# Kernel tuning notes

Measured on AMD Instinct MI355X. Metric: run time of the kernel, lower is better.

The kernel has to match this reference:

```python
import jax, jax.numpy as jnp
import numpy as np

# Instant-NGP style multiresolution hash grid config
L = 16                      # n_levels
F = 2                       # n_feat_per_entry
LEVEL_SIZE = 524288         # 2^19 hash entries per level
RES = np.array([16, 22, 30, 42, 58, 80, 111, 154, 212, 294, 406, 561, 776, 1072, 1482, 2048], np.int32)
OFFSETS = (np.arange(L + 1) * LEVEL_SIZE).astype(np.int32)
PRIMES = np.array([1, 2654435761, 805459861], dtype=np.uint32)  # spatial hash primes
# 8 corner offsets of a voxel, (8, 3) in {0,1}
CORNERS = np.array([[(c >> d) & 1 for d in range(3)] for c in range(8)], np.int32)


def setup_inputs() -> dict:
    key = jax.random.key(0)
    k1, k2 = jax.random.split(key)
    B = 1000000
    xyz = jax.random.uniform(k1, (B, 3), dtype=jnp.float32)  # points in [0,1)
    embeddings = jax.random.normal(k2, (int(OFFSETS[-1]), F), dtype=jnp.float32) * 0.01
    return {
        'xyz': xyz,
        'embeddings': embeddings,
        'min_xyz': jnp.zeros((3,), jnp.float32),
        'max_xyz': jnp.ones((3,), jnp.float32),
    }


def _encode(xyz, embeddings, min_xyz, max_xyz):
    B = xyz.shape[0]
    norm = (xyz - min_xyz) / (max_xyz - min_xyz)          # (B, 3) in [0,1] if inside grid
    valid = jnp.all((norm >= 0.0) & (norm <= 1.0), axis=-1)  # (B,)
    corners = jnp.asarray(CORNERS)                        # (8, 3)
    primes = jnp.asarray(PRIMES)
    outs = []
    for l in range(L):  # fixed small loop over levels (different resolution per level)
        r = int(RES[l])
        pos = norm * (r - 1)                              # (B, 3) grid coords
        fi = jnp.clip(jnp.floor(pos).astype(jnp.int32), 0, r - 2)  # (B, 3) base corner
        frac = pos - fi.astype(pos.dtype)                 # (B, 3) trilinear fraction
        c = fi[:, None, :] + corners[None, :, :]          # (B, 8, 3) corner coords
        # trilinear interpolation weights, (B, 8)
        w = jnp.prod(jnp.where(corners[None] == 1, frac[:, None, :], 1.0 - frac[:, None, :]), axis=-1)
        # spatial hash into this level's table slice
        cu = c.astype(jnp.uint32)
        h = (cu[..., 0] * primes[0]) ^ (cu[..., 1] * primes[1]) ^ (cu[..., 2] * primes[2])
        lvl_size = jnp.uint32(int(OFFSETS[l + 1] - OFFSETS[l]))
        idx = (h % lvl_size).astype(jnp.int32) + int(OFFSETS[l])   # (B, 8) global entry ids
        feats = embeddings[idx]                           # (B, 8, F) irregular gather
        outs.append(jnp.sum(w[..., None] * feats, axis=1))  # (B, F)
    out = jnp.stack(outs, axis=1).reshape(B, L * F)       # (B, L*F)
    return jnp.where(valid[:, None], out, jnp.zeros((), out.dtype))


def reference(xyz, embeddings, min_xyz, max_xyz):
    return _encode(xyz, embeddings, min_xyz, max_xyz)
```

## Files before the change

kernel.cpp:

```cpp
#include <hip/hip_runtime.h>
#include <hip/hip_fp16.h>
#include <stdint.h>

#define NLEVELS 16
#define BLOCK 256
#define NPT 2

#define P1 2654435761u
#define P2 805459861u
#define HMASK 0x7FFFFu

__device__ __host__ constexpr int DRES(int l) {
    constexpr int r[6] = {16, 22, 30, 42, 58, 80};
    return r[l];
}
__device__ __host__ constexpr uint32_t QOFF(int l) {
    constexpr uint32_t o[7] = {0, 3600, 13302, 38532, 109134, 297576, 796856};
    return o[l];
}
#define QUAD_ENTRIES 796856u
#define HASH16_ENTRIES (10u << 19)
#define HASH16_BYTES ((size_t)HASH16_ENTRIES * 4)
#define QUAD_BYTES   ((size_t)QUAD_ENTRIES * 16)
#define PREP_TOTAL   (HASH16_ENTRIES + QUAD_ENTRIES)


__device__ __forceinline__ uint32_t fetch_pack(const float* __restrict__ emb,
                                               int l, uint32_t x, uint32_t y, uint32_t z)
{
    const uint32_t h = (x ^ (y * P1) ^ (z * P2)) & HMASK;
    const float2 v = *reinterpret_cast<const float2*>(emb + (((size_t)l << 19) + h) * 2);
    __half2 hv = __floats2half2_rn(v.x, v.y);
    return *reinterpret_cast<uint32_t*>(&hv);
}

template <int L>
__device__ __forceinline__ void qbuild(uint32_t rel, const float* __restrict__ emb,
                                       uint4* __restrict__ quad)
{
    constexpr int r = DRES(L);
    constexpr int rW = r - 1;
    const uint32_t fz = rel / (uint32_t)(rW * rW);
    const uint32_t rem = rel - fz * (uint32_t)(rW * rW);
    const uint32_t fy = rem / (uint32_t)rW;
    const uint32_t fx = rem - fy * (uint32_t)rW;
    uint4 q;
    q.x = fetch_pack(emb, L, fx,     fy,     fz);
    q.y = fetch_pack(emb, L, fx + 1, fy,     fz);
    q.z = fetch_pack(emb, L, fx,     fy + 1, fz);
    q.w = fetch_pack(emb, L, fx + 1, fy + 1, fz);
    quad[QOFF(L) + rel] = q;
}

__global__ __launch_bounds__(BLOCK) void prep_kernel(
    const float* __restrict__ emb,
    uint32_t* __restrict__ tab16,
    uint4* __restrict__ quad)
{
    const uint32_t i = blockIdx.x * BLOCK + threadIdx.x;
    if (i < HASH16_ENTRIES) {
        const float2 v = *reinterpret_cast<const float2*>(
            emb + (((size_t)(6u << 19)) + i) * 2);
        __half2 hv = __floats2half2_rn(v.x, v.y);
        __builtin_nontemporal_store(*reinterpret_cast<uint32_t*>(&hv), &tab16[i]);
    } else if (i < PREP_TOTAL) {
        const uint32_t j = i - HASH16_ENTRIES;
        if      (j < QOFF(1)) qbuild<0>(j - QOFF(0), emb, quad);
        else if (j < QOFF(2)) qbuild<1>(j - QOFF(1), emb, quad);
        else if (j < QOFF(3)) qbuild<2>(j - QOFF(2), emb, quad);
        else if (j < QOFF(4)) qbuild<3>(j - QOFF(3), emb, quad);
        else if (j < QOFF(5)) qbuild<4>(j - QOFF(4), emb, quad);
        else                  qbuild<5>(j - QOFF(5), emb, quad);
    }
}


struct PointCtx { float nx, ny, nz; bool valid; };

__device__ __forceinline__ PointCtx make_ctx(const float* __restrict__ xyz, int pt, int B,
                                             float mn0, float mn1, float mn2,
                                             float inv0, float inv1, float inv2)
{
    PointCtx P;
    P.nx = P.ny = P.nz = 0.0f;
    P.valid = false;
    if (pt < B) {
        const float x = xyz[3 * pt + 0];
        const float y = xyz[3 * pt + 1];
        const float z = xyz[3 * pt + 2];
        P.nx = (x - mn0) * inv0;
        P.ny = (y - mn1) * inv1;
        P.nz = (z - mn2) * inv2;
        P.valid = (P.nx >= 0.0f) && (P.nx <= 1.0f) &&
                  (P.ny >= 0.0f) && (P.ny <= 1.0f) &&
                  (P.nz >= 0.0f) && (P.nz <= 1.0f);
    }
    return P;
}

__device__ __forceinline__ void frac_setup(const PointCtx& P, int r,
                                           int& fx, int& fy, int& fz,
                                           float& wx0, float& wx1,
                                           float& wy0, float& wy1,
                                           float& wz0, float& wz1)
{
    const float rm1 = (float)(r - 1);
    const float px = P.nx * rm1, py = P.ny * rm1, pz = P.nz * rm1;
    fx = (int)floorf(px); fx = min(max(fx, 0), r - 2);
    fy = (int)floorf(py); fy = min(max(fy, 0), r - 2);
    fz = (int)floorf(pz); fz = min(max(fz, 0), r - 2);
    wx1 = px - (float)fx; wx0 = 1.0f - wx1;
    wy1 = py - (float)fy; wy0 = 1.0f - wy1;
    wz1 = pz - (float)fz; wz0 = 1.0f - wz1;
}

__device__ __forceinline__ float2 h2f(uint32_t e)
{
    return __half22float2(*reinterpret_cast<const __half2*>(&e));
}

__device__ __forceinline__ float2 quad_encode(const PointCtx& P, int r, uint32_t qoff,
                                              const uint4* __restrict__ quad)
{
    int fx, fy, fz; float wx0, wx1, wy0, wy1, wz0, wz1;
    frac_setup(P, r, fx, fy, fz, wx0, wx1, wy0, wy1, wz0, wz1);
    const int rW = r - 1;
    const uint32_t base = qoff + (uint32_t)(fx + fy * rW + fz * rW * rW);
    const uint4 q0 = quad[base];
    const uint4 q1 = quad[base + (uint32_t)(rW * rW)];

    const float2 a0 = h2f(q0.x), b0 = h2f(q0.y), c0 = h2f(q0.z), d0 = h2f(q0.w);
    const float2 a1 = h2f(q1.x), b1 = h2f(q1.y), c1 = h2f(q1.z), d1 = h2f(q1.w);

    const float p0x = wy0 * (wx0 * a0.x + wx1 * b0.x) + wy1 * (wx0 * c0.x + wx1 * d0.x);
    const float p0y = wy0 * (wx0 * a0.y + wx1 * b0.y) + wy1 * (wx0 * c0.y + wx1 * d0.y);
    const float p1x = wy0 * (wx0 * a1.x + wx1 * b1.x) + wy1 * (wx0 * c1.x + wx1 * d1.x);
    const float p1y = wy0 * (wx0 * a1.y + wx1 * b1.y) + wy1 * (wx0 * c1.y + wx1 * d1.y);

    float2 o;
    o.x = P.valid ? (wz0 * p0x + wz1 * p1x) : 0.0f;
    o.y = P.valid ? (wz0 * p0y + wz1 * p1y) : 0.0f;
    return o;
}

__device__ __forceinline__ float2 hash_encode(const PointCtx& P, int r,
                                              const uint32_t* __restrict__ lt)
{
    int fx, fy, fz; float wx0, wx1, wy0, wy1, wz0, wz1;
    frac_setup(P, r, fx, fy, fz, wx0, wx1, wy0, wy1, wz0, wz1);
    const uint32_t hx0 = (uint32_t)fx;
    const uint32_t hy0 = (uint32_t)fy * P1, hy1 = hy0 + P1;
    const uint32_t hz0 = (uint32_t)fz * P2, hz1 = hz0 + P2;
    const bool oddx = (fx & 1) != 0;

    uint32_t i0[4];
    uint2 pr[4];
    #pragma unroll
    for (int yz = 0; yz < 4; ++yz) {
        const uint32_t rest = ((yz & 1) ? hy1 : hy0) ^ ((yz & 2) ? hz1 : hz0);
        i0[yz] = (hx0 ^ rest) & HMASK;
        pr[yz] = *reinterpret_cast<const uint2*>(lt + (i0[yz] & ~1u));
    }
    uint32_t e1x[4] = {0, 0, 0, 0};
    if (oddx) {
        #pragma unroll
        for (int yz = 0; yz < 4; ++yz) {
            const uint32_t rest = ((yz & 1) ? hy1 : hy0) ^ ((yz & 2) ? hz1 : hz0);
            e1x[yz] = lt[((hx0 + 1u) ^ rest) & HMASK];
        }
    }

    float acc0 = 0.0f, acc1 = 0.0f;
    #pragma unroll
    for (int yz = 0; yz < 4; ++yz) {
        const float wyz = ((yz & 1) ? wy1 : wy0) * ((yz & 2) ? wz1 : wz0);
        const uint32_t eA = (i0[yz] & 1u) ? pr[yz].y : pr[yz].x;
        const uint32_t eB0 = (i0[yz] & 1u) ? pr[yz].x : pr[yz].y;
        const uint32_t eB = oddx ? e1x[yz] : eB0;
        const float2 cA = h2f(eA);
        const float2 cB = h2f(eB);
        acc0 += wyz * (wx0 * cA.x + wx1 * cB.x);
        acc1 += wyz * (wx0 * cA.y + wx1 * cB.y);
    }
    float2 o;
    o.x = P.valid ? acc0 : 0.0f;
    o.y = P.valid ? acc1 : 0.0f;
    return o;
}

__device__ __forceinline__ void nt_store_f2h(uint32_t* p, float2 v)
{
    __half2 h = __floats2half2_rn(v.x, v.y);
    __builtin_nontemporal_store(*reinterpret_cast<uint32_t*>(&h), p);
}

__global__ __launch_bounds__(BLOCK, 4) void gather_mega_kernel(
    const float* __restrict__ xyz,
    const uint32_t* __restrict__ tab16,
    const uint4* __restrict__ quad,
    const float* __restrict__ minv,
    const float* __restrict__ maxv,
    uint32_t* __restrict__ slab,
    int B, int blocks2)
{
    constexpr int HRES[10] = {111, 154, 212, 294, 406, 561, 776, 1072, 1482, 2048};

    const int seg = blockIdx.x / blocks2;
    const int blk = blockIdx.x - seg * blocks2;

    const int t = threadIdx.x;
    const int p0 = blk * (NPT * BLOCK) + t;
    const int p1 = p0 + BLOCK;

    const float mn0 = minv[0], mn1 = minv[1], mn2 = minv[2];
    const float inv0 = 1.0f / (maxv[0] - mn0);
    const float inv1 = 1.0f / (maxv[1] - mn1);
    const float inv2 = 1.0f / (maxv[2] - mn2);

    const PointCtx A  = make_ctx(xyz, p0, B, mn0, mn1, mn2, inv0, inv1, inv2);
    const PointCtx Bc = make_ctx(xyz, p1, B, mn0, mn1, mn2, inv0, inv1, inv2);

    if (seg == 0) {
        #pragma unroll
        for (int l = 0; l < 5; ++l) {
            const float2 o0 = quad_encode(A,  DRES(l), QOFF(l), quad);
            const float2 o1 = quad_encode(Bc, DRES(l), QOFF(l), quad);
            if (p0 < B) nt_store_f2h(&slab[(size_t)l * B + p0], o0);
            if (p1 < B) nt_store_f2h(&slab[(size_t)l * B + p1], o1);
        }
    } else if (seg == 1) {
        const float2 o0 = quad_encode(A,  DRES(5), QOFF(5), quad);
        const float2 o1 = quad_encode(Bc, DRES(5), QOFF(5), quad);
        if (p0 < B) nt_store_f2h(&slab[(size_t)5 * B + p0], o0);
        if (p1 < B) nt_store_f2h(&slab[(size_t)5 * B + p1], o1);
    } else {
        const int l = seg + 4;
        const int r = HRES[seg - 2];
        const uint32_t* __restrict__ lt = tab16 + ((size_t)(l - 6) << 19);
        const float2 o0 = hash_encode(A,  r, lt);
        const float2 o1 = hash_encode(Bc, r, lt);
        if (p0 < B) nt_store_f2h(&slab[(size_t)l * B + p0], o0);
        if (p1 < B) nt_store_f2h(&slab[(size_t)l * B + p1], o1);
    }
}

__global__ __launch_bounds__(BLOCK) void transpose_kernel(
    const uint32_t* __restrict__ slab,
    float* __restrict__ out,
    int B)
{
    __shared__ float s[32][BLOCK + 1];
    const int t = threadIdx.x;
    const int pt = blockIdx.x * BLOCK + t;

    #pragma unroll
    for (int l = 0; l < NLEVELS; ++l) {
        float2 v = make_float2(0.0f, 0.0f);
        if (pt < B) {
            const uint32_t bits = __builtin_nontemporal_load(&slab[(size_t)l * B + pt]);
            v = h2f(bits);
        }
        s[2 * l + 0][t] = v.x;
        s[2 * l + 1][t] = v.y;
    }
    __syncthreads();

    const size_t chunk = (size_t)blockIdx.x * (BLOCK * 32);
    const size_t total = (size_t)B * 32;
    #pragma unroll
    for (int k = 0; k < 32; ++k) {
        const int flat = k * BLOCK + t;
        const int p = flat >> 5;
        const int c = flat & 31;
        const size_t g = chunk + (size_t)flat;
        if (g < total) __builtin_nontemporal_store(s[c][p], &out[g]);
    }
}

__global__ __launch_bounds__(BLOCK) void hashgrid_fused_kernel(
    const float* __restrict__ xyz,
    const float* __restrict__ emb,
    const float* __restrict__ minv,
    const float* __restrict__ maxv,
    float* __restrict__ out,
    int B)
{
    constexpr int RES[NLEVELS] = {16, 22, 30, 42, 58, 80, 111, 154,
                                  212, 294, 406, 561, 776, 1072, 1482, 2048};
    __shared__ float s[32][BLOCK + 1];
    const int t = threadIdx.x;
    const int pt = blockIdx.x * BLOCK + t;

    const float mn0 = minv[0], mn1 = minv[1], mn2 = minv[2];
    const float inv0 = 1.0f / (maxv[0] - mn0);
    const float inv1 = 1.0f / (maxv[1] - mn1);
    const float inv2 = 1.0f / (maxv[2] - mn2);

    const PointCtx P = make_ctx(xyz, pt, B, mn0, mn1, mn2, inv0, inv1, inv2);

    #pragma unroll
    for (int l = 0; l < NLEVELS; ++l) {
        int fx, fy, fz; float wx0, wx1, wy0, wy1, wz0, wz1;
        frac_setup(P, RES[l], fx, fy, fz, wx0, wx1, wy0, wy1, wz0, wz1);
        const uint32_t hx0 = (uint32_t)fx, hx1 = hx0 + 1u;
        const uint32_t hy0 = (uint32_t)fy * P1, hy1 = hy0 + P1;
        const uint32_t hz0 = (uint32_t)fz * P2, hz1 = hz0 + P2;
        const float* __restrict__ lemb = emb + ((size_t)l << 20);
        float acc0 = 0.0f, acc1 = 0.0f;
        #pragma unroll
        for (int k = 0; k < 8; ++k) {
            const uint32_t h = (((k & 1) ? hx1 : hx0) ^
                                ((k & 2) ? hy1 : hy0) ^
                                ((k & 4) ? hz1 : hz0)) & HMASK;
            const float2 f = *reinterpret_cast<const float2*>(lemb + ((size_t)h << 1));
            const float w = ((k & 1) ? wx1 : wx0) * ((k & 2) ? wy1 : wy0) * ((k & 4) ? wz1 : wz0);
            acc0 = fmaf(w, f.x, acc0);
            acc1 = fmaf(w, f.y, acc1);
        }
        s[2 * l + 0][t] = P.valid ? acc0 : 0.0f;
        s[2 * l + 1][t] = P.valid ? acc1 : 0.0f;
    }
    __syncthreads();
    const size_t chunk = (size_t)blockIdx.x * (BLOCK * 32);
    const size_t total = (size_t)B * 32;
    #pragma unroll
    for (int k = 0; k < 32; ++k) {
        const int flat = k * BLOCK + t;
        const int p = flat >> 5;
        const int c = flat & 31;
        const size_t g = chunk + (size_t)flat;
        if (g < total) out[g] = s[c][p];
    }
}

extern "C" void kernel_launch(void* const* d_in, const int* in_sizes, int n_in,
                              void* d_out, int out_size, void* d_ws, size_t ws_size,
                              hipStream_t stream) {
    const float* xyz = (const float*)d_in[0];
    const float* emb = (const float*)d_in[1];
    const float* mn  = (const float*)d_in[2];
    const float* mx  = (const float*)d_in[3];
    float* out = (float*)d_out;

    const int B = in_sizes[0] / 3;
    const int blocks1 = (B + BLOCK - 1) / BLOCK;
    const int blocks2 = (B + NPT * BLOCK - 1) / (NPT * BLOCK);

    const size_t slab_bytes = (size_t)NLEVELS * (size_t)B * 4;
    const size_t ws_needed = slab_bytes + HASH16_BYTES + QUAD_BYTES;

    if (ws_size >= ws_needed) {
        uint32_t* slab  = (uint32_t*)d_ws;
        uint32_t* tab16 = (uint32_t*)((char*)d_ws + slab_bytes);
        uint4*    quad  = (uint4*)((char*)d_ws + slab_bytes + HASH16_BYTES);

        hipLaunchKernelGGL(prep_kernel,
                           dim3((PREP_TOTAL + BLOCK - 1) / BLOCK), dim3(BLOCK),
                           0, stream, emb, tab16, quad);

        hipLaunchKernelGGL(gather_mega_kernel, dim3(12 * blocks2), dim3(BLOCK), 0, stream,
                           xyz, tab16, quad, mn, mx, slab, B, blocks2);

        hipLaunchKernelGGL(transpose_kernel, dim3(blocks1), dim3(BLOCK), 0, stream,
                           slab, out, B);
    } else {
        hipLaunchKernelGGL(hashgrid_fused_kernel, dim3(blocks1), dim3(BLOCK), 0, stream,
                           xyz, emb, mn, mx, out, B);
    }
}
```

Measured before the change: 368.5 us.

## Replace quad-packed dense tables with x-pair duplicated tables and simplify hash gather

Dense levels 0-5 now store one 8-byte x-pair record per voxel (two fp16x2 corner features) instead of 16-byte quads covering the x/y face. Interpolation therefore needs four 8-byte loads per point instead of two 16-byte loads, and the precomputed table is about half the size. The hash levels drop the paired-load and odd-x trick in favour of eight plain 4-byte gathers. The smaller dense table cuts prep writes, at the cost of more load instructions in the gather kernel.

```diff
diff --git a/kernel.cpp b/kernel.cpp
--- a/kernel.cpp
+++ b/kernel.cpp
@@ -14,15 +14,15 @@
     constexpr int r[6] = {16, 22, 30, 42, 58, 80};
     return r[l];
 }
-__device__ __host__ constexpr uint32_t QOFF(int l) {
-    constexpr uint32_t o[7] = {0, 3600, 13302, 38532, 109134, 297576, 796856};
+__device__ __host__ constexpr uint32_t DOFF(int l) {
+    constexpr uint32_t o[7] = {0, 4096, 14744, 41744, 115832, 310944, 822944};
     return o[l];
 }
-#define QUAD_ENTRIES 796856u
+#define DENSE_ENTRIES 822944u
 #define HASH16_ENTRIES (10u << 19)
 #define HASH16_BYTES ((size_t)HASH16_ENTRIES * 4)
-#define QUAD_BYTES   ((size_t)QUAD_ENTRIES * 16)
-#define PREP_TOTAL   (HASH16_ENTRIES + QUAD_ENTRIES)
+#define DUP_BYTES    ((size_t)DENSE_ENTRIES * 8)
+#define PREP_TOTAL   (HASH16_ENTRIES + DENSE_ENTRIES)
 
 
 __device__ __forceinline__ uint32_t fetch_pack(const float* __restrict__ emb,
@@ -34,28 +34,10 @@
     return *reinterpret_cast<uint32_t*>(&hv);
 }
 
-template <int L>
-__device__ __forceinline__ void qbuild(uint32_t rel, const float* __restrict__ emb,
-                                       uint4* __restrict__ quad)
-{
-    constexpr int r = DRES(L);
-    constexpr int rW = r - 1;
-    const uint32_t fz = rel / (uint32_t)(rW * rW);
-    const uint32_t rem = rel - fz * (uint32_t)(rW * rW);
-    const uint32_t fy = rem / (uint32_t)rW;
-    const uint32_t fx = rem - fy * (uint32_t)rW;
-    uint4 q;
-    q.x = fetch_pack(emb, L, fx,     fy,     fz);
-    q.y = fetch_pack(emb, L, fx + 1, fy,     fz);
-    q.z = fetch_pack(emb, L, fx,     fy + 1, fz);
-    q.w = fetch_pack(emb, L, fx + 1, fy + 1, fz);
-    quad[QOFF(L) + rel] = q;
-}
-
 __global__ __launch_bounds__(BLOCK) void prep_kernel(
     const float* __restrict__ emb,
     uint32_t* __restrict__ tab16,
-    uint4* __restrict__ quad)
+    uint2* __restrict__ dup)
 {
     const uint32_t i = blockIdx.x * BLOCK + threadIdx.x;
     if (i < HASH16_ENTRIES) {
@@ -65,12 +47,20 @@
         __builtin_nontemporal_store(*reinterpret_cast<uint32_t*>(&hv), &tab16[i]);
     } else if (i < PREP_TOTAL) {
         const uint32_t j = i - HASH16_ENTRIES;
-        if      (j < QOFF(1)) qbuild<0>(j - QOFF(0), emb, quad);
-        else if (j < QOFF(2)) qbuild<1>(j - QOFF(1), emb, quad);
-        else if (j < QOFF(3)) qbuild<2>(j - QOFF(2), emb, quad);
-        else if (j < QOFF(4)) qbuild<3>(j - QOFF(3), emb, quad);
-        else if (j < QOFF(5)) qbuild<4>(j - QOFF(4), emb, quad);
-        else                  qbuild<5>(j - QOFF(5), emb, quad);
+        int l = 0;
+        #pragma unroll
+        for (int q = 1; q < 6; ++q) if (j >= DOFF(q)) l = q;
+        const int r = DRES(l);
+        const uint32_t rel = j - DOFF(l);
+        const uint32_t z = rel / (uint32_t)(r * r);
+        const uint32_t rem = rel - z * (uint32_t)(r * r);
+        const uint32_t y = rem / (uint32_t)r;
+        const uint32_t x = rem - y * (uint32_t)r;
+        const uint32_t x1 = min(x + 1u, (uint32_t)(r - 1));
+        uint2 e;
+        e.x = fetch_pack(emb, l, x,  y, z);
+        e.y = fetch_pack(emb, l, x1, y, z);
+        dup[j] = e;
     }
 }
 
@@ -119,68 +109,42 @@
     return __half22float2(*reinterpret_cast<const __half2*>(&e));
 }
 
-__device__ __forceinline__ float2 quad_encode(const PointCtx& P, int r, uint32_t qoff,
-                                              const uint4* __restrict__ quad)
+__device__ __forceinline__ float2 dup_encode(const PointCtx& P, int r, uint32_t off,
+                                             const uint2* __restrict__ dup)
 {
     int fx, fy, fz; float wx0, wx1, wy0, wy1, wz0, wz1;
     frac_setup(P, r, fx, fy, fz, wx0, wx1, wy0, wy1, wz0, wz1);
-    const int rW = r - 1;
-    const uint32_t base = qoff + (uint32_t)(fx + fy * rW + fz * rW * rW);
-    const uint4 q0 = quad[base];
-    const uint4 q1 = quad[base + (uint32_t)(rW * rW)];
-
-    const float2 a0 = h2f(q0.x), b0 = h2f(q0.y), c0 = h2f(q0.z), d0 = h2f(q0.w);
-    const float2 a1 = h2f(q1.x), b1 = h2f(q1.y), c1 = h2f(q1.z), d1 = h2f(q1.w);
-
-    const float p0x = wy0 * (wx0 * a0.x + wx1 * b0.x) + wy1 * (wx0 * c0.x + wx1 * d0.x);
-    const float p0y = wy0 * (wx0 * a0.y + wx1 * b0.y) + wy1 * (wx0 * c0.y + wx1 * d0.y);
-    const float p1x = wy0 * (wx0 * a1.x + wx1 * b1.x) + wy1 * (wx0 * c1.x + wx1 * d1.x);
-    const float p1y = wy0 * (wx0 * a1.y + wx1 * b1.y) + wy1 * (wx0 * c1.y + wx1 * d1.y);
-
-    float2 o;
-    o.x = P.valid ? (wz0 * p0x + wz1 * p1x) : 0.0f;
-    o.y = P.valid ? (wz0 * p0y + wz1 * p1y) : 0.0f;
-    return o;
-}
-
-__device__ __forceinline__ float2 hash_encode(const PointCtx& P, int r,
-                                              const uint32_t* __restrict__ lt)
-{
-    int fx, fy, fz; float wx0, wx1, wy0, wy1, wz0, wz1;
-    frac_setup(P, r, fx, fy, fz, wx0, wx1, wy0, wy1, wz0, wz1);
-    const uint32_t hx0 = (uint32_t)fx;
-    const uint32_t hy0 = (uint32_t)fy * P1, hy1 = hy0 + P1;
-    const uint32_t hz0 = (uint32_t)fz * P2, hz1 = hz0 + P2;
-    const bool oddx = (fx & 1) != 0;
-
-    uint32_t i0[4];
-    uint2 pr[4];
-    #pragma unroll
-    for (int yz = 0; yz < 4; ++yz) {
-        const uint32_t rest = ((yz & 1) ? hy1 : hy0) ^ ((yz & 2) ? hz1 : hz0);
-        i0[yz] = (hx0 ^ rest) & HMASK;
-        pr[yz] = *reinterpret_cast<const uint2*>(lt + (i0[yz] & ~1u));
-    }
-    uint32_t e1x[4] = {0, 0, 0, 0};
-    if (oddx) {
-        #pragma unroll
-        for (int yz = 0; yz < 4; ++yz) {
-            const uint32_t rest = ((yz & 1) ? hy1 : hy0) ^ ((yz & 2) ? hz1 : hz0);
-            e1x[yz] = lt[((hx0 + 1u) ^ rest) & HMASK];
-        }
-    }
+    const uint32_t base = off + (uint32_t)(fx + fy * r + fz * r * r);
+
+    const uint2 q00 = dup[base];
+    const uint2 q10 = dup[base + (uint32_t)r];
+    const uint2 q01 = dup[base + (uint32_t)(r * r)];
+    const uint2 q11 = dup[base + (uint32_t)(r + r * r)];
 
     float acc0 = 0.0f, acc1 = 0.0f;
-    #pragma unroll
-    for (int yz = 0; yz < 4; ++yz) {
-        const float wyz = ((yz & 1) ? wy1 : wy0) * ((yz & 2) ? wz1 : wz0);
-        const uint32_t eA = (i0[yz] & 1u) ? pr[yz].y : pr[yz].x;
-        const uint32_t eB0 = (i0[yz] & 1u) ? pr[yz].x : pr[yz].y;
-        const uint32_t eB = oddx ? e1x[yz] : eB0;
-        const float2 cA = h2f(eA);
-        const float2 cB = h2f(eB);
-        acc0 += wyz * (wx0 * cA.x + wx1 * cB.x);
-        acc1 += wyz * (wx0 * cA.y + wx1 * cB.y);
+    {
+        const float w = wy0 * wz0;
+        const float2 a = h2f(q00.x), b = h2f(q00.y);
+        acc0 += w * (wx0 * a.x + wx1 * b.x);
+        acc1 += w * (wx0 * a.y + wx1 * b.y);
+    }
+    {
+        const float w = wy1 * wz0;
+        const float2 a = h2f(q10.x), b = h2f(q10.y);
+        acc0 += w * (wx0 * a.x + wx1 * b.x);
+        acc1 += w * (wx0 * a.y + wx1 * b.y);
+    }
+    {
+        const float w = wy0 * wz1;
+        const float2 a = h2f(q01.x), b = h2f(q01.y);
+        acc0 += w * (wx0 * a.x + wx1 * b.x);
+        acc1 += w * (wx0 * a.y + wx1 * b.y);
+    }
+    {
+        const float w = wy1 * wz1;
+        const float2 a = h2f(q11.x), b = h2f(q11.y);
+        acc0 += w * (wx0 * a.x + wx1 * b.x);
+        acc1 += w * (wx0 * a.y + wx1 * b.y);
     }
     float2 o;
     o.x = P.valid ? acc0 : 0.0f;
@@ -188,6 +152,37 @@
     return o;
 }
 
+__device__ __forceinline__ float2 hash_encode(const PointCtx& P, int r,
+                                              const uint32_t* __restrict__ lt)
+{
+    int fx, fy, fz; float wx0, wx1, wy0, wy1, wz0, wz1;
+    frac_setup(P, r, fx, fy, fz, wx0, wx1, wy0, wy1, wz0, wz1);
+    const uint32_t hx0 = (uint32_t)fx,      hx1 = hx0 + 1u;
+    const uint32_t hy0 = (uint32_t)fy * P1, hy1 = hy0 + P1;
+    const uint32_t hz0 = (uint32_t)fz * P2, hz1 = hz0 + P2;
+
+    uint32_t e[8];
+    #pragma unroll
+    for (int k = 0; k < 8; ++k) {
+        const uint32_t h = (((k & 1) ? hx1 : hx0) ^
+                            ((k & 2) ? hy1 : hy0) ^
+                            ((k & 4) ? hz1 : hz0)) & HMASK;
+        e[k] = lt[h];
+    }
+    float acc0 = 0.0f, acc1 = 0.0f;
+    #pragma unroll
+    for (int k = 0; k < 8; ++k) {
+        const float w = ((k & 1) ? wx1 : wx0) * ((k & 2) ? wy1 : wy0) * ((k & 4) ? wz1 : wz0);
+        const float2 f = h2f(e[k]);
+        acc0 = fmaf(w, f.x, acc0);
+        acc1 = fmaf(w, f.y, acc1);
+    }
+    float2 o;
+    o.x = P.valid ? acc0 : 0.0f;
+    o.y = P.valid ? acc1 : 0.0f;
+    return o;
+}
+
 __device__ __forceinline__ void nt_store_f2h(uint32_t* p, float2 v)
 {
     __half2 h = __floats2half2_rn(v.x, v.y);
@@ -197,7 +192,7 @@
 __global__ __launch_bounds__(BLOCK, 4) void gather_mega_kernel(
     const float* __restrict__ xyz,
     const uint32_t* __restrict__ tab16,
-    const uint4* __restrict__ quad,
+    const uint2* __restrict__ dup,
     const float* __restrict__ minv,
     const float* __restrict__ maxv,
     uint32_t* __restrict__ slab,
@@ -223,14 +218,14 @@
     if (seg == 0) {
         #pragma unroll
         for (int l = 0; l < 5; ++l) {
-            const float2 o0 = quad_encode(A,  DRES(l), QOFF(l), quad);
-            const float2 o1 = quad_encode(Bc, DRES(l), QOFF(l), quad);
+            const float2 o0 = dup_encode(A,  DRES(l), DOFF(l), dup);
+            const float2 o1 = dup_encode(Bc, DRES(l), DOFF(l), dup);
             if (p0 < B) nt_store_f2h(&slab[(size_t)l * B + p0], o0);
             if (p1 < B) nt_store_f2h(&slab[(size_t)l * B + p1], o1);
         }
     } else if (seg == 1) {
-        const float2 o0 = quad_encode(A,  DRES(5), QOFF(5), quad);
-        const float2 o1 = quad_encode(Bc, DRES(5), QOFF(5), quad);
+        const float2 o0 = dup_encode(A,  DRES(5), DOFF(5), dup);
+        const float2 o1 = dup_encode(Bc, DRES(5), DOFF(5), dup);
         if (p0 < B) nt_store_f2h(&slab[(size_t)5 * B + p0], o0);
         if (p1 < B) nt_store_f2h(&slab[(size_t)5 * B + p1], o1);
     } else {
@@ -347,19 +342,19 @@
     const int blocks2 = (B + NPT * BLOCK - 1) / (NPT * BLOCK);
 
     const size_t slab_bytes = (size_t)NLEVELS * (size_t)B * 4;
-    const size_t ws_needed = slab_bytes + HASH16_BYTES + QUAD_BYTES;
+    const size_t ws_needed = slab_bytes + HASH16_BYTES + DUP_BYTES;
 
     if (ws_size >= ws_needed) {
         uint32_t* slab  = (uint32_t*)d_ws;
         uint32_t* tab16 = (uint32_t*)((char*)d_ws + slab_bytes);
-        uint4*    quad  = (uint4*)((char*)d_ws + slab_bytes + HASH16_BYTES);
+        uint2*    dup   = (uint2*)((char*)d_ws + slab_bytes + HASH16_BYTES);
 
         hipLaunchKernelGGL(prep_kernel,
                            dim3((PREP_TOTAL + BLOCK - 1) / BLOCK), dim3(BLOCK),
-                           0, stream, emb, tab16, quad);
+                           0, stream, emb, tab16, dup);
 
         hipLaunchKernelGGL(gather_mega_kernel, dim3(12 * blocks2), dim3(BLOCK), 0, stream,
-                           xyz, tab16, quad, mn, mx, slab, B, blocks2);
+                           xyz, tab16, dup, mn, mx, slab, B, blocks2);
 
         hipLaunchKernelGGL(transpose_kernel, dim3(blocks1), dim3(BLOCK), 0, stream,
                            slab, out, B);
```

After: 330.5 us. 10.3% less time.
